# Optimization experiments

Measured on AMD Instinct MI355X. Metric: run time of the kernel, lower is better.

## Reference

```python
import jax, jax.numpy as jnp
import numpy as np

N_NODES = 100000
N_EDGES = 1600000
F_IN = 128
EMB = 128
HEADS = 4
D_HEAD = EMB // HEADS
HIDDEN = 256
BATCH = 2048
CANDS = 16  # distractors + 1


def setup_inputs() -> dict:
    key = jax.random.key(0)
    ks = jax.random.split(key, 10)
    message = jax.random.normal(ks[0], (BATCH, HIDDEN), jnp.float32)
    x = jax.random.normal(ks[1], (N_NODES, F_IN), jnp.float32)
    edge_index = jax.random.randint(ks[2], (2, N_EDGES), 0, N_NODES, jnp.int64)
    indices = jax.random.randint(ks[3], (BATCH * CANDS,), 0, N_NODES, jnp.int64)
    s = 1.0 / np.sqrt(F_IN)
    W = jax.random.normal(ks[4], (F_IN, HEADS, D_HEAD), jnp.float32) * s
    att_src = jax.random.normal(ks[5], (HEADS, D_HEAD), jnp.float32) * s
    att_dst = jax.random.normal(ks[6], (HEADS, D_HEAD), jnp.float32) * s
    bias = jnp.zeros((EMB,), jnp.float32)
    fc_w = jax.random.normal(ks[7], (EMB, HIDDEN), jnp.float32) / np.sqrt(HIDDEN)
    fc_b = jnp.zeros((EMB,), jnp.float32)
    return {"message": message, "x": x, "edge_index": edge_index, "indices": indices,
            "W": W, "att_src": att_src, "att_dst": att_dst, "bias": bias,
            "fc_w": fc_w, "fc_b": fc_b}


def _gat(x, edge_index, W, att_src, att_dst, bias):
    N = x.shape[0]
    loops = jnp.arange(N, dtype=edge_index.dtype)
    src = jnp.concatenate([edge_index[0], loops])  # self-loops (PyG default)
    dst = jnp.concatenate([edge_index[1], loops])
    Wx = jnp.einsum('nf,fhd->nhd', x, W)                      # [N,H,D]
    a_s = (Wx * att_src).sum(-1)                              # [N,H]
    a_d = (Wx * att_dst).sum(-1)
    e = jax.nn.leaky_relu(a_s[src] + a_d[dst], 0.2)           # [E,H]
    m = jax.ops.segment_max(e, dst, num_segments=N)           # segment softmax
    ex = jnp.exp(e - m[dst])
    den = jax.ops.segment_sum(ex, dst, num_segments=N)
    alpha = ex / den[dst]
    out = jax.ops.segment_sum(alpha[:, :, None] * Wx[src], dst, num_segments=N)
    return out.reshape(N, -1) + bias                          # [N, H*D]


def reference(message, x, edge_index, indices, W, att_src, att_dst, bias, fc_w, fc_b):
    h = _gat(x, edge_index, W, att_src, att_dst, bias)        # [N, EMB]
    B = message.shape[0]
    emb = h[indices].reshape(B, -1, h.shape[-1])              # [B,C,EMB]
    msg = message @ fc_w.T + fc_b                             # [B,EMB]
    dots = jnp.einsum('bce,be->bc', emb, msg)                 # bmm scoring
    amax = jnp.abs(dots).max()
    tie = ((jnp.abs(dots) - amax) < 1e-10).astype(dots.dtype)
    noise = jax.random.normal(jax.random.key(42), dots.shape, dots.dtype)
    dots = dots + tie * amax * 1e-5 * noise
    return jax.nn.log_softmax(dots, axis=1)
```

## Files before the change

kernel.cpp:

```cpp
#include <hip/hip_runtime.h>
#include <stdint.h>
#include <stddef.h>

#define N_NODES 100000
#define N_EDGES 1600000
#define F_IN 128
#define EMB 128
#define HEADS 4
#define D_HEAD 32
#define HIDDEN 256
#define BATCH 2048
#define CANDS 16
#define MAXNEED 32768
#define WXBLOCKS 391
#define WTROWS 144
#define STR 136

typedef __attribute__((ext_vector_type(8))) short v8s;
typedef __attribute__((ext_vector_type(4))) float v4f;

__device__ __forceinline__ unsigned short f2bs(float f) {
  unsigned int u = __builtin_bit_cast(unsigned int, f);
  u = (u + 0x7fffu + ((u >> 16) & 1u)) >> 16;
  return (unsigned short)u;
}
__device__ __forceinline__ float bs2f(unsigned int s) {
  unsigned int u = (s & 0xffffu) << 16;
  return __builtin_bit_cast(float, u);
}

__global__ __launch_bounds__(256) void k_prep(const float* __restrict__ W,
                                              const float* __restrict__ att_src,
                                              const float* __restrict__ att_dst,
                                              unsigned short* __restrict__ Wtp,
                                              const int* __restrict__ idx,
                                              int* __restrict__ mark,
                                              int* __restrict__ nidx,
                                              int* __restrict__ nlist,
                                              int* __restrict__ nw_cnt) {
  int i = blockIdx.x * 256 + threadIdx.x;
  if (i < 128 * STR) {
    int r = i / STR, c = i - r * STR;
    Wtp[i] = (c < 128) ? f2bs(W[c * 128 + r]) : (unsigned short)0;
  } else if (i < WTROWS * STR) {
    int ii = i - 128 * STR;
    int r = ii / STR, c = ii - r * STR;
    unsigned short v = 0;
    if (c < 128 && r < 8) {
      const float* att = (r < 4) ? att_src : att_dst;
      int hh = r & 3;
      float s = 0.f;
#pragma unroll
      for (int d = 0; d < 32; ++d) s += W[c * 128 + hh * 32 + d] * att[hh * 32 + d];
      v = f2bs(s);
    }
    Wtp[i] = v;
  }
  if (i < BATCH * CANDS) {
    int v = idx[i];
    if (atomicAdd(&mark[v], 1) == 0) {
      int p = atomicAdd(nw_cnt, 1);
      nidx[v] = p + 1;
      nlist[p] = v;
    }
  }
}

__global__ __launch_bounds__(256) void k_wx(const float* __restrict__ x,
                                            const unsigned short* __restrict__ Wtp,
                                            unsigned short* __restrict__ Wx,
                                            float* __restrict__ a_s,
                                            float* __restrict__ a_d) {
  __shared__ unsigned short wt[WTROWS * STR];
  __shared__ unsigned short xs[64 * STR];
  int tid = threadIdx.x;

  {
    const uint4* s = (const uint4*)Wtp;
    uint4* d = (uint4*)wt;
#pragma unroll
    for (int it = 0; it < 10; ++it) {
      int i = it * 256 + tid;
      if (i < WTROWS * STR / 8) d[i] = s[i];
    }
  }

  int w = tid >> 6, lane = tid & 63;
  int m = lane & 15, quad = lane >> 4;

  for (int chunk = 0; chunk < 4; ++chunk) {
    int rbase = blockIdx.x * 256 + chunk * 64;

    float4 f[8];
#pragma unroll
    for (int it = 0; it < 4; ++it) {
      int cid = it * 256 + tid;
      int row = cid >> 4, c = cid & 15;
      int gr = rbase + row;
      if (gr >= N_NODES) gr = N_NODES - 1;
      const float4* gp = (const float4*)(x + (size_t)gr * 128 + c * 8);
      f[2 * it] = gp[0];
      f[2 * it + 1] = gp[1];
    }
#pragma unroll
    for (int it = 0; it < 4; ++it) {
      int cid = it * 256 + tid;
      int row = cid >> 4, c = cid & 15;
      float4 f0 = f[2 * it], f1 = f[2 * it + 1];
      v8s a;
      a[0] = (short)f2bs(f0.x); a[1] = (short)f2bs(f0.y);
      a[2] = (short)f2bs(f0.z); a[3] = (short)f2bs(f0.w);
      a[4] = (short)f2bs(f1.x); a[5] = (short)f2bs(f1.y);
      a[6] = (short)f2bs(f1.z); a[7] = (short)f2bs(f1.w);
      *(v8s*)(&xs[row * STR + c * 8]) = a;
    }
    __syncthreads();

    v8s afrag[4];
#pragma unroll
    for (int t = 0; t < 4; ++t)
      afrag[t] = *(const v8s*)(&xs[(w * 16 + m) * STR + t * 32 + quad * 8]);

    v4f acc[9];
#pragma unroll
    for (int nt = 0; nt < 9; ++nt) {
      v4f a0 = {0.f, 0.f, 0.f, 0.f};
      const unsigned short* brow = wt + (size_t)(nt * 16 + m) * STR;
#pragma unroll
      for (int t = 0; t < 4; ++t) {
        v8s b = *(const v8s*)(brow + t * 32 + quad * 8);
        a0 = __builtin_amdgcn_mfma_f32_16x16x32_bf16(afrag[t], b, a0, 0, 0, 0);
      }
      acc[nt] = a0;
    }

#pragma unroll
    for (int r = 0; r < 4; ++r) {
      int orow = rbase + w * 16 + quad * 4 + r;
      if (orow < N_NODES) {
        if (m < 4) a_s[(size_t)orow * 4 + m] = acc[8][r];
        else if (m < 8) a_d[(size_t)orow * 4 + m - 4] = acc[8][r];
      }
    }

    __syncthreads();
#pragma unroll
    for (int nt = 0; nt < 8; ++nt)
#pragma unroll
      for (int r = 0; r < 4; ++r)
        xs[(w * 16 + quad * 4 + r) * STR + nt * 16 + m] = f2bs(acc[nt][r]);
    asm volatile("s_waitcnt lgkmcnt(0)" ::: "memory");
#pragma unroll
    for (int j = 0; j < 4; ++j) {
      int fr = 4 * j + (lane >> 4);
      int fc = (lane & 15) * 8;
      int grow = rbase + w * 16 + fr;
      v8s v = *(const v8s*)(&xs[(w * 16 + fr) * STR + fc]);
      if (grow < N_NODES) *(v8s*)(&Wx[(size_t)grow * 128 + fc]) = v;
    }
    __syncthreads();
  }
}

__global__ __launch_bounds__(256) void k_scatter(const int* __restrict__ ei,
                                                 const int* __restrict__ nidx,
                                                 int* __restrict__ cnt,
                                                 int* __restrict__ srclist) {
  int e = blockIdx.x * 256 + threadIdx.x;
  if (e >= N_EDGES) return;
  int dst = ei[N_EDGES + e];
  int ni = nidx[dst];
  if (!ni) return;
  ni--;
  int pos = atomicAdd(&cnt[ni], 1);
  if (pos < 64) srclist[ni * 64 + pos] = ei[e];
}

__global__ __launch_bounds__(256) void k_agg(const float* __restrict__ a_s,
                                             const float* __restrict__ a_d,
                                             const unsigned short* __restrict__ Wx,
                                             const int* __restrict__ nlist,
                                             const int* __restrict__ nw_cnt,
                                             const int* __restrict__ cnt,
                                             const int* __restrict__ srclist,
                                             const int* __restrict__ ei,
                                             const float* __restrict__ bias,
                                             unsigned short* __restrict__ hout) {
  __shared__ int sS[16][64];
  __shared__ float sW[16][64 * 4];
  int w = threadIdx.x >> 6, lane = threadIdx.x & 63;
  int q = lane >> 4, li = lane & 15;
  int wq = w * 4 + q;
  int wid = (blockIdx.x * 4 + w) * 4 + q;
  bool act = wid < nw_cnt[0];
  int dst = 0, degRaw = 0, deg = 0;
  float4 ad4 = {0.f, 0.f, 0.f, 0.f};
  float4 dsum = {0.f, 0.f, 0.f, 0.f};
  if (act) {
    dst = nlist[wid];
    degRaw = cnt[wid];
    deg = degRaw < 64 ? degRaw : 64;
    ad4 = *(const float4*)(a_d + (size_t)dst * 4);
    for (int t = li; t < deg; t += 16) {
      int sv = srclist[wid * 64 + t];
      float4 as = *(const float4*)(a_s + (size_t)sv * 4);
      float e0 = as.x + ad4.x; e0 = e0 > 0.f ? e0 : 0.2f * e0;
      float e1 = as.y + ad4.y; e1 = e1 > 0.f ? e1 : 0.2f * e1;
      float e2 = as.z + ad4.z; e2 = e2 > 0.f ? e2 : 0.2f * e2;
      float e3 = as.w + ad4.w; e3 = e3 > 0.f ? e3 : 0.2f * e3;
      float4 w4;
      w4.x = __expf(e0); w4.y = __expf(e1);
      w4.z = __expf(e2); w4.w = __expf(e3);
      sS[wq][t] = sv;
      *(float4*)(&sW[wq][t * 4]) = w4;
      dsum.x += w4.x; dsum.y += w4.y; dsum.z += w4.z; dsum.w += w4.w;
    }
  }
  __syncthreads();
  if (!act) return;

#pragma unroll
  for (int o = 8; o >= 1; o >>= 1) {
    dsum.x += __shfl_xor(dsum.x, o);
    dsum.y += __shfl_xor(dsum.y, o);
    dsum.z += __shfl_xor(dsum.z, o);
    dsum.w += __shfl_xor(dsum.w, o);
  }

  int hh = li >> 2;
  float4 as4 = *(const float4*)(a_s + (size_t)dst * 4);
  float s0 = as4.x + ad4.x; s0 = s0 > 0.f ? s0 : 0.2f * s0;
  float s1 = as4.y + ad4.y; s1 = s1 > 0.f ? s1 : 0.2f * s1;
  float s2 = as4.z + ad4.z; s2 = s2 > 0.f ? s2 : 0.2f * s2;
  float s3 = as4.w + ad4.w; s3 = s3 > 0.f ? s3 : 0.2f * s3;
  float w0 = __expf(s0), w1 = __expf(s1), w2 = __expf(s2), w3 = __expf(s3);
  float wSelf = hh < 2 ? (hh == 0 ? w0 : w1) : (hh == 2 ? w2 : w3);
  float denE = hh < 2 ? (hh == 0 ? dsum.x : dsum.y) : (hh == 2 ? dsum.z : dsum.w);
  float den = denE + wSelf;

  float acc[8];
  {
    uint4 u = *(const uint4*)(Wx + (size_t)dst * 128 + li * 8);
    acc[0] = wSelf * bs2f(u.x); acc[1] = wSelf * bs2f(u.x >> 16);
    acc[2] = wSelf * bs2f(u.y); acc[3] = wSelf * bs2f(u.y >> 16);
    acc[4] = wSelf * bs2f(u.z); acc[5] = wSelf * bs2f(u.z >> 16);
    acc[6] = wSelf * bs2f(u.w); acc[7] = wSelf * bs2f(u.w >> 16);
  }

  if (degRaw > 64) {
    float adH = hh < 2 ? (hh == 0 ? ad4.x : ad4.y) : (hh == 2 ? ad4.z : ad4.w);
    den = wSelf;
    for (int e = 0; e < N_EDGES; ++e) {
      if (ei[N_EDGES + e] == dst) {
        int sv = ei[e];
        float ash = a_s[(size_t)sv * 4 + hh];
        float ee = ash + adH; ee = ee > 0.f ? ee : 0.2f * ee;
        float wA = __expf(ee);
        den += wA;
        uint4 u = *(const uint4*)(Wx + (size_t)sv * 128 + li * 8);
        acc[0] += wA * bs2f(u.x); acc[1] += wA * bs2f(u.x >> 16);
        acc[2] += wA * bs2f(u.y); acc[3] += wA * bs2f(u.y >> 16);
        acc[4] += wA * bs2f(u.z); acc[5] += wA * bs2f(u.z >> 16);
        acc[6] += wA * bs2f(u.w); acc[7] += wA * bs2f(u.w >> 16);
      }
    }
  } else {
#pragma unroll 4
    for (int j = 0; j < deg; ++j) {
      int s = sS[wq][j];
      float wA = sW[wq][j * 4 + hh];
      uint4 u = *(const uint4*)(Wx + (size_t)s * 128 + li * 8);
      acc[0] += wA * bs2f(u.x); acc[1] += wA * bs2f(u.x >> 16);
      acc[2] += wA * bs2f(u.y); acc[3] += wA * bs2f(u.y >> 16);
      acc[4] += wA * bs2f(u.z); acc[5] += wA * bs2f(u.z >> 16);
      acc[6] += wA * bs2f(u.w); acc[7] += wA * bs2f(u.w >> 16);
    }
  }

  float inv = 1.0f / den;
  float4 b0 = *(const float4*)(bias + li * 8);
  float4 b1 = *(const float4*)(bias + li * 8 + 4);
  uint4 o;
  o.x = (unsigned int)f2bs(acc[0] * inv + b0.x)
      | ((unsigned int)f2bs(acc[1] * inv + b0.y) << 16);
  o.y = (unsigned int)f2bs(acc[2] * inv + b0.z)
      | ((unsigned int)f2bs(acc[3] * inv + b0.w) << 16);
  o.z = (unsigned int)f2bs(acc[4] * inv + b1.x)
      | ((unsigned int)f2bs(acc[5] * inv + b1.y) << 16);
  o.w = (unsigned int)f2bs(acc[6] * inv + b1.z)
      | ((unsigned int)f2bs(acc[7] * inv + b1.w) << 16);
  *(uint4*)(hout + (size_t)dst * 128 + li * 8) = o;
}

__global__ __launch_bounds__(256) void k_msgscore(const float* __restrict__ message,
                                                  const float* __restrict__ fc_w,
                                                  const float* __restrict__ fc_b,
                                                  const unsigned short* __restrict__ h,
                                                  const int* __restrict__ indices,
                                                  float* __restrict__ out) {
  __shared__ float Sm[8][256];
  __shared__ float red[8 * 128];
  __shared__ float sp[128];
  int tid = threadIdx.x;
  int b0 = blockIdx.x * 8;
  for (int i = tid; i < 8 * 256; i += 256)
    Sm[i >> 8][i & 255] = message[(size_t)b0 * 256 + i];
  __syncthreads();
  int e = tid & 127, half = tid >> 7;
  float acc[8];
#pragma unroll
  for (int r = 0; r < 8; ++r) acc[r] = 0.f;
  const float* wrow = fc_w + (size_t)e * 256 + half * 128;
  for (int k = 0; k < 128; k += 4) {
    float4 w4 = *(const float4*)(wrow + k);
#pragma unroll
    for (int r = 0; r < 8; ++r) {
      float4 m4 = *(const float4*)(&Sm[r][half * 128 + k]);
      acc[r] += m4.x * w4.x + m4.y * w4.y + m4.z * w4.z + m4.w * w4.w;
    }
  }
  __syncthreads();
  if (half == 0) {
#pragma unroll
    for (int r = 0; r < 8; ++r) red[r * 128 + e] = acc[r];
  }
  __syncthreads();
  if (half == 1) {
#pragma unroll
    for (int r = 0; r < 8; ++r) red[r * 128 + e] += acc[r];
  }
  __syncthreads();
  for (int i = tid; i < 1024; i += 256) red[i] += fc_b[i & 127];
  __syncthreads();

  int r = (tid & 127) >> 4, c = tid & 15;
  int idx = indices[(b0 + r) * 16 + c];
  const unsigned short* hr = h + (size_t)idx * 128 + half * 64;
  const float* mr = red + r * 128 + half * 64;
  float dot = 0.f;
#pragma unroll
  for (int k = 0; k < 64; k += 8) {
    uint4 qv = *(const uint4*)(hr + k);
    float4 m0 = *(const float4*)(mr + k);
    float4 m1 = *(const float4*)(mr + k + 4);
    dot += bs2f(qv.x) * m0.x + bs2f(qv.x >> 16) * m0.y
         + bs2f(qv.y) * m0.z + bs2f(qv.y >> 16) * m0.w
         + bs2f(qv.z) * m1.x + bs2f(qv.z >> 16) * m1.y
         + bs2f(qv.w) * m1.z + bs2f(qv.w >> 16) * m1.w;
  }
  if (half == 1) sp[tid - 128] = dot;
  __syncthreads();
  if (half == 0) {
    dot += sp[tid];
    float mx = dot;
#pragma unroll
    for (int o = 1; o < 16; o <<= 1) mx = fmaxf(mx, __shfl_xor(mx, o));
    float ex = __expf(dot - mx);
    float sum = ex;
#pragma unroll
    for (int o = 1; o < 16; o <<= 1) sum += __shfl_xor(sum, o);
    float lse = mx + __logf(sum);
    out[(b0 + r) * 16 + c] = dot - lse;
  }
}

extern "C" void kernel_launch(void* const* d_in, const int* in_sizes, int n_in,
                              void* d_out, int out_size, void* d_ws, size_t ws_size,
                              hipStream_t stream) {
  (void)in_sizes; (void)n_in; (void)out_size; (void)ws_size;
  const float* message = (const float*)d_in[0];
  const float* x       = (const float*)d_in[1];
  const int*   ei      = (const int*)d_in[2];
  const int*   indices = (const int*)d_in[3];
  const float* W       = (const float*)d_in[4];
  const float* att_src = (const float*)d_in[5];
  const float* att_dst = (const float*)d_in[6];
  const float* bias    = (const float*)d_in[7];
  const float* fc_w    = (const float*)d_in[8];
  const float* fc_b    = (const float*)d_in[9];
  float* out = (float*)d_out;

  char* p = (char*)d_ws;
  auto alloc = [&](size_t bytes) -> char* {
    char* r = p;
    p += (bytes + 255) & ~(size_t)255;
    return r;
  };
  unsigned short* Wx = (unsigned short*)alloc((size_t)N_NODES * 128 * 2);
  unsigned short* h  = (unsigned short*)alloc((size_t)N_NODES * 128 * 2);
  float* a_s = (float*)alloc((size_t)N_NODES * 4 * 4);
  float* a_d = (float*)alloc((size_t)N_NODES * 4 * 4);
  unsigned short* Wtp = (unsigned short*)alloc((size_t)WTROWS * STR * 2);
  int* mark      = (int*)alloc((size_t)N_NODES * 4);
  int* nidx      = (int*)alloc((size_t)N_NODES * 4);
  int* cnt       = (int*)alloc((size_t)MAXNEED * 4);
  int* nw_cnt    = (int*)alloc(4);
  int* nlist     = (int*)alloc((size_t)MAXNEED * 4);
  int* srclist   = (int*)alloc((size_t)MAXNEED * 64 * 4);

  hipMemsetAsync(mark, 0, (size_t)((char*)nlist - (char*)mark), stream);

  k_prep<<<128, 256, 0, stream>>>(W, att_src, att_dst, Wtp, indices, mark, nidx, nlist, nw_cnt);
  k_wx<<<WXBLOCKS, 256, 0, stream>>>(x, Wtp, Wx, a_s, a_d);
  k_scatter<<<N_EDGES / 256, 256, 0, stream>>>(ei, nidx, cnt, srclist);
  k_agg<<<MAXNEED / 16, 256, 0, stream>>>(a_s, a_d, Wx, nlist, nw_cnt, cnt, srclist, ei, bias, h);
  k_msgscore<<<BATCH / 8, 256, 0, stream>>>(message, fc_w, fc_b, h, indices, out);
}
```

Baseline: 192.1 us.

## Replace dedup atomics with last-writer slot map and fuse message FC into scatter

Needed-node tracking drops the zero-initialised mark array, the atomic compaction list and the host memset. Each candidate slot now writes its own index into nidx, and a slot counts as the owner when idx[nidx[dst]] == dst, so nidx needs no clearing. The message FC projection moves into the edge-scatter launch as extra blocks, leaving the scoring kernel to only gather and dot. The cost is doing aggregation over 32768 slots with duplicates filtered by an ownership check, plus an extra global round-trip for the projected message.

```diff
diff --git a/kernel.cpp b/kernel.cpp
--- a/kernel.cpp
+++ b/kernel.cpp
@@ -11,7 +11,7 @@
 #define HIDDEN 256
 #define BATCH 2048
 #define CANDS 16
-#define MAXNEED 32768
+#define NSLOTS 32768
 #define WXBLOCKS 391
 #define WTROWS 144
 #define STR 136
@@ -34,10 +34,8 @@
                                               const float* __restrict__ att_dst,
                                               unsigned short* __restrict__ Wtp,
                                               const int* __restrict__ idx,
-                                              int* __restrict__ mark,
                                               int* __restrict__ nidx,
-                                              int* __restrict__ nlist,
-                                              int* __restrict__ nw_cnt) {
+                                              int* __restrict__ cnt) {
   int i = blockIdx.x * 256 + threadIdx.x;
   if (i < 128 * STR) {
     int r = i / STR, c = i - r * STR;
@@ -56,13 +54,64 @@
     }
     Wtp[i] = v;
   }
-  if (i < BATCH * CANDS) {
-    int v = idx[i];
-    if (atomicAdd(&mark[v], 1) == 0) {
-      int p = atomicAdd(nw_cnt, 1);
-      nidx[v] = p + 1;
-      nlist[p] = v;
-    }
+  if (i < NSLOTS) {
+    cnt[i] = 0;
+    nidx[idx[i]] = i;
+  }
+}
+
+__global__ __launch_bounds__(256) void k_scatmsg(const int* __restrict__ ei,
+                                                 const int* __restrict__ idx,
+                                                 const int* __restrict__ nidx,
+                                                 int* __restrict__ cnt,
+                                                 int* __restrict__ srclist,
+                                                 const float* __restrict__ message,
+                                                 const float* __restrict__ fc_w,
+                                                 const float* __restrict__ fc_b,
+                                                 float* __restrict__ msg) {
+  __shared__ float Sm[8][256];
+  __shared__ float red[8 * 128];
+  int tid = threadIdx.x;
+  if (blockIdx.x < 256) {
+    int b0 = blockIdx.x * 8;
+    for (int i = tid; i < 8 * 256; i += 256)
+      Sm[i >> 8][i & 255] = message[(size_t)b0 * 256 + i];
+    __syncthreads();
+    int e = tid & 127, half = tid >> 7;
+    float acc[8];
+#pragma unroll
+    for (int r = 0; r < 8; ++r) acc[r] = 0.f;
+    const float* wrow = fc_w + (size_t)e * 256 + half * 128;
+    for (int k = 0; k < 128; k += 4) {
+      float4 w4 = *(const float4*)(wrow + k);
+#pragma unroll
+      for (int r = 0; r < 8; ++r) {
+        float4 m4 = *(const float4*)(&Sm[r][half * 128 + k]);
+        acc[r] += m4.x * w4.x + m4.y * w4.y + m4.z * w4.z + m4.w * w4.w;
+      }
+    }
+    __syncthreads();
+    if (half == 0) {
+#pragma unroll
+      for (int r = 0; r < 8; ++r) red[r * 128 + e] = acc[r];
+    }
+    __syncthreads();
+    if (half == 1) {
+#pragma unroll
+      for (int r = 0; r < 8; ++r) red[r * 128 + e] += acc[r];
+    }
+    __syncthreads();
+    for (int i = tid; i < 1024; i += 256)
+      msg[(size_t)b0 * 128 + i] = red[i] + fc_b[i & 127];
+  } else {
+    int e = (blockIdx.x - 256) * 256 + tid;
+    if (e >= N_EDGES) return;
+    int dst = ei[N_EDGES + e];
+    unsigned int ni = (unsigned int)nidx[dst];
+    if (ni >= NSLOTS) return;
+    if (idx[ni] != dst) return;
+    int pos = atomicAdd(&cnt[ni], 1);
+    if (pos < 64) srclist[ni * 64 + pos] = ei[e];
   }
 }
 
@@ -162,25 +211,11 @@
   }
 }
 
-__global__ __launch_bounds__(256) void k_scatter(const int* __restrict__ ei,
-                                                 const int* __restrict__ nidx,
-                                                 int* __restrict__ cnt,
-                                                 int* __restrict__ srclist) {
-  int e = blockIdx.x * 256 + threadIdx.x;
-  if (e >= N_EDGES) return;
-  int dst = ei[N_EDGES + e];
-  int ni = nidx[dst];
-  if (!ni) return;
-  ni--;
-  int pos = atomicAdd(&cnt[ni], 1);
-  if (pos < 64) srclist[ni * 64 + pos] = ei[e];
-}
-
 __global__ __launch_bounds__(256) void k_agg(const float* __restrict__ a_s,
                                              const float* __restrict__ a_d,
                                              const unsigned short* __restrict__ Wx,
-                                             const int* __restrict__ nlist,
-                                             const int* __restrict__ nw_cnt,
+                                             const int* __restrict__ idx,
+                                             const int* __restrict__ nidx,
                                              const int* __restrict__ cnt,
                                              const int* __restrict__ srclist,
                                              const int* __restrict__ ei,
@@ -192,12 +227,12 @@
   int q = lane >> 4, li = lane & 15;
   int wq = w * 4 + q;
   int wid = (blockIdx.x * 4 + w) * 4 + q;
-  bool act = wid < nw_cnt[0];
-  int dst = 0, degRaw = 0, deg = 0;
+  int dst = idx[wid];
+  bool act = (nidx[dst] == wid);
+  int degRaw = 0, deg = 0;
   float4 ad4 = {0.f, 0.f, 0.f, 0.f};
   float4 dsum = {0.f, 0.f, 0.f, 0.f};
   if (act) {
-    dst = nlist[wid];
     degRaw = cnt[wid];
     deg = degRaw < 64 ? degRaw : 64;
     ad4 = *(const float4*)(a_d + (size_t)dst * 4);
@@ -292,51 +327,21 @@
   *(uint4*)(hout + (size_t)dst * 128 + li * 8) = o;
 }
 
-__global__ __launch_bounds__(256) void k_msgscore(const float* __restrict__ message,
-                                                  const float* __restrict__ fc_w,
-                                                  const float* __restrict__ fc_b,
-                                                  const unsigned short* __restrict__ h,
-                                                  const int* __restrict__ indices,
-                                                  float* __restrict__ out) {
-  __shared__ float Sm[8][256];
-  __shared__ float red[8 * 128];
+__global__ __launch_bounds__(256) void k_score(const float* __restrict__ msg,
+                                               const unsigned short* __restrict__ h,
+                                               const int* __restrict__ indices,
+                                               float* __restrict__ out) {
+  __shared__ float Sm[8 * 128];
   __shared__ float sp[128];
   int tid = threadIdx.x;
   int b0 = blockIdx.x * 8;
-  for (int i = tid; i < 8 * 256; i += 256)
-    Sm[i >> 8][i & 255] = message[(size_t)b0 * 256 + i];
+  for (int i = tid; i < 1024; i += 256) Sm[i] = msg[(size_t)b0 * 128 + i];
   __syncthreads();
-  int e = tid & 127, half = tid >> 7;
-  float acc[8];
-#pragma unroll
-  for (int r = 0; r < 8; ++r) acc[r] = 0.f;
-  const float* wrow = fc_w + (size_t)e * 256 + half * 128;
-  for (int k = 0; k < 128; k += 4) {
-    float4 w4 = *(const float4*)(wrow + k);
-#pragma unroll
-    for (int r = 0; r < 8; ++r) {
-      float4 m4 = *(const float4*)(&Sm[r][half * 128 + k]);
-      acc[r] += m4.x * w4.x + m4.y * w4.y + m4.z * w4.z + m4.w * w4.w;
-    }
-  }
-  __syncthreads();
-  if (half == 0) {
-#pragma unroll
-    for (int r = 0; r < 8; ++r) red[r * 128 + e] = acc[r];
-  }
-  __syncthreads();
-  if (half == 1) {
-#pragma unroll
-    for (int r = 0; r < 8; ++r) red[r * 128 + e] += acc[r];
-  }
-  __syncthreads();
-  for (int i = tid; i < 1024; i += 256) red[i] += fc_b[i & 127];
-  __syncthreads();
-
-  int r = (tid & 127) >> 4, c = tid & 15;
-  int idx = indices[(b0 + r) * 16 + c];
-  const unsigned short* hr = h + (size_t)idx * 128 + half * 64;
-  const float* mr = red + r * 128 + half * 64;
+
+  int r = (tid & 127) >> 4, c = tid & 15, half = tid >> 7;
+  int id = indices[(b0 + r) * 16 + c];
+  const unsigned short* hr = h + (size_t)id * 128 + half * 64;
+  const float* mr = Sm + r * 128 + half * 64;
   float dot = 0.f;
 #pragma unroll
   for (int k = 0; k < 64; k += 8) {
@@ -391,18 +396,15 @@
   float* a_s = (float*)alloc((size_t)N_NODES * 4 * 4);
   float* a_d = (float*)alloc((size_t)N_NODES * 4 * 4);
   unsigned short* Wtp = (unsigned short*)alloc((size_t)WTROWS * STR * 2);
-  int* mark      = (int*)alloc((size_t)N_NODES * 4);
   int* nidx      = (int*)alloc((size_t)N_NODES * 4);
-  int* cnt       = (int*)alloc((size_t)MAXNEED * 4);
-  int* nw_cnt    = (int*)alloc(4);
-  int* nlist     = (int*)alloc((size_t)MAXNEED * 4);
-  int* srclist   = (int*)alloc((size_t)MAXNEED * 64 * 4);
-
-  hipMemsetAsync(mark, 0, (size_t)((char*)nlist - (char*)mark), stream);
-
-  k_prep<<<128, 256, 0, stream>>>(W, att_src, att_dst, Wtp, indices, mark, nidx, nlist, nw_cnt);
+  int* cnt       = (int*)alloc((size_t)NSLOTS * 4);
+  int* srclist   = (int*)alloc((size_t)NSLOTS * 64 * 4);
+  float* msg     = (float*)alloc((size_t)BATCH * 128 * 4);
+
+  k_prep<<<128, 256, 0, stream>>>(W, att_src, att_dst, Wtp, indices, nidx, cnt);
+  k_scatmsg<<<256 + N_EDGES / 256, 256, 0, stream>>>(ei, indices, nidx, cnt, srclist,
+                                                     message, fc_w, fc_b, msg);
   k_wx<<<WXBLOCKS, 256, 0, stream>>>(x, Wtp, Wx, a_s, a_d);
-  k_scatter<<<N_EDGES / 256, 256, 0, stream>>>(ei, nidx, cnt, srclist);
-  k_agg<<<MAXNEED / 16, 256, 0, stream>>>(a_s, a_d, Wx, nlist, nw_cnt, cnt, srclist, ei, bias, h);
-  k_msgscore<<<BATCH / 8, 256, 0, stream>>>(message, fc_w, fc_b, h, indices, out);
-}
+  k_agg<<<NSLOTS / 16, 256, 0, stream>>>(a_s, a_d, Wx, indices, nidx, cnt, srclist, ei, bias, h);
+  k_score<<<BATCH / 8, 256, 0, stream>>>(msg, h, indices, out);
+}
```

Measured after the change: 179.1 us. 6.8% less time.
